# Performance work log

Measured on AMD Instinct MI355X. Metric: run time of the kernel, lower is better.

Reference implementation:

```python
import jax, jax.numpy as jnp
import numpy as np

# Model dims (GatedAttentionLayer of Qwen3.5 ANE hybrid stack)
C = 2048      # hidden_size
H = 16        # num_attention_heads
HK = 4        # num_key_value_heads
D = 128       # head_dim
ROT = 32      # rotary_dim = head_dim * partial_rotary_factor (0.25)
S = 1024      # sequence length (prefill)
CTX = 1024    # kv cache context length
N_ATTN = 6    # number of full-attention layers -> kv_cache leading dim 2*N_ATTN
EPS = 1e-6
ROPE_THETA = 1e7


def _rotate_half(x):
    h = x.shape[-1] // 2
    return jnp.concatenate([-x[..., h:], x[..., :h]], axis=-1)


def _rms_norm(x, w, eps=EPS):
    # Qwen3.5 convention: stored weight is (w - 1), applied as (1 + weight)
    r = jax.lax.rsqrt(jnp.mean(x * x, axis=-1, keepdims=True) + eps)
    return x * r * (1.0 + w)


def setup_inputs() -> dict:
    key = jax.random.key(0)
    ks = jax.random.split(key, 6)
    hidden_states = jax.random.normal(ks[0], (1, C, 1, S), jnp.float32)
    q_proj_w = jax.random.normal(ks[1], (H * 2 * D, C), jnp.float32) * 0.02  # q + gate
    k_proj_w = jax.random.normal(ks[2], (HK * D, C), jnp.float32) * 0.02
    v_proj_w = jax.random.normal(ks[3], (HK * D, C), jnp.float32) * 0.02
    o_proj_w = jax.random.normal(ks[4], (C, H * D), jnp.float32) * 0.02
    q_norm_w = jnp.zeros((D,), jnp.float32)
    k_norm_w = jnp.zeros((D,), jnp.float32)
    kv_cache = jnp.zeros((2 * N_ATTN, HK, CTX, D), jnp.float32)
    position_ids = jnp.arange(S, dtype=jnp.int32)
    # causal mask: 0 on/below diagonal, -1e9 above
    causal_mask = jnp.where(
        jnp.arange(CTX)[None, :] <= jnp.arange(S)[:, None], 0.0, -1e9
    ).astype(jnp.float32)[None, None]  # [1,1,S,CTX]
    # RoPE tables over rotary_dim
    inv_freq = 1.0 / (ROPE_THETA ** (jnp.arange(0, ROT, 2, dtype=jnp.float32) / ROT))
    t = jnp.arange(CTX, dtype=jnp.float32)
    freqs = jnp.outer(t, inv_freq)          # [CTX, ROT//2]
    emb = jnp.concatenate([freqs, freqs], -1)  # [CTX, ROT]
    cos_cached = jnp.cos(emb)
    sin_cached = jnp.sin(emb)
    return dict(hidden_states=hidden_states, q_proj_w=q_proj_w, k_proj_w=k_proj_w,
                v_proj_w=v_proj_w, o_proj_w=o_proj_w, q_norm_w=q_norm_w,
                k_norm_w=k_norm_w, kv_cache=kv_cache, causal_mask=causal_mask,
                position_ids=position_ids, cos_cached=cos_cached,
                sin_cached=sin_cached, attn_layer_idx=0)


def reference(hidden_states, q_proj_w, k_proj_w, v_proj_w, o_proj_w,
              q_norm_w, k_norm_w, kv_cache, causal_mask, position_ids,
              cos_cached, sin_cached, attn_layer_idx):
    x = hidden_states[0, :, 0, :]                     # [C, S]
    q_raw = q_proj_w @ x                              # [H*2D, S]  (1x1 Conv2d == GEMM)
    qg = q_raw.reshape(H, 2 * D, S)
    q = jnp.transpose(qg[:, :D, :], (0, 2, 1))        # [H, S, D]
    gate = jnp.transpose(qg[:, D:, :], (0, 2, 1))     # [H, S, D]
    k = jnp.transpose((k_proj_w @ x).reshape(HK, D, S), (0, 2, 1))  # [HK, S, D]
    v = jnp.transpose((v_proj_w @ x).reshape(HK, D, S), (0, 2, 1))  # [HK, S, D]

    q = _rms_norm(q, q_norm_w)
    k = _rms_norm(k, k_norm_w)

    cos = cos_cached[position_ids]   # [S, ROT]
    sin = sin_cached[position_ids]

    def rope(t):
        rot, pas = t[..., :ROT], t[..., ROT:]
        rot = rot * cos + _rotate_half(rot) * sin
        return jnp.concatenate([rot, pas], axis=-1)

    q, k = rope(q), rope(k)

    # prefill cache write at pos_start = position_ids[0]
    k_idx = 2 * attn_layer_idx
    v_idx = k_idx + 1
    pos_start = position_ids[0]
    kv_cache = jax.lax.dynamic_update_slice(kv_cache, k[None], (k_idx, 0, pos_start, 0))
    kv_cache = jax.lax.dynamic_update_slice(kv_cache, v[None], (v_idx, 0, pos_start, 0))

    g = H // HK  # GQA repeat (expand+reshape == contiguous repeat)
    k_full = jnp.repeat(kv_cache[k_idx], g, axis=0)   # [H, CTX, D]
    v_full = jnp.repeat(kv_cache[v_idx], g, axis=0)   # [H, CTX, D]

    scale = D ** -0.5
    attn = jnp.einsum('hsd,htd->hst', q, k_full) * scale + causal_mask[0]
    attn = jax.nn.softmax(attn, axis=-1)
    out = jnp.einsum('hst,htd->hsd', attn, v_full)    # [H, S, D]
    out = out * jax.nn.sigmoid(gate)
    out = jnp.transpose(out, (0, 2, 1)).reshape(H * D, S)
    output = (o_proj_w @ out)[None, :, None, :]       # [1, C, 1, S]
    return output
```

## Files before the change

### kernel.cpp

```cpp
#include <hip/hip_runtime.h>
#include <cstdint>

#define S_LEN 1024
#define C_DIM 2048
#define NH    16
#define NHK   4
#define HD    128
#define ROT   32
#define SCALE 0.08838834764831845f

typedef __bf16 bf16x8 __attribute__((ext_vector_type(8)));
typedef float floatx4 __attribute__((ext_vector_type(4)));
typedef float floatx16 __attribute__((ext_vector_type(16)));
typedef unsigned short ushortx8 __attribute__((ext_vector_type(8)));

__device__ __forceinline__ unsigned short f2bf(float f) {
  union { float f; uint32_t u; } x; x.f = f;
  uint32_t r = (x.u + 0x7fffu + ((x.u >> 16) & 1u)) >> 16;
  return (unsigned short)r;
}
__device__ __forceinline__ float bf2f(unsigned short v) {
  union { uint32_t u; float f; } x; x.u = (uint32_t)v << 16; return x.f;
}

__device__ __forceinline__ void async_copy16(const unsigned short* g, unsigned short* l) {
  __builtin_amdgcn_global_load_lds(
      (const __attribute__((address_space(1))) void*)g,
      (__attribute__((address_space(3))) void*)l,
      16, 0, 0);
}

#define WAIT_VM(N) asm volatile("s_waitcnt vmcnt(" #N ")" ::: "memory")

__device__ __forceinline__ void bar_lds_only() {
  asm volatile("s_waitcnt lgkmcnt(0)" ::: "memory");
  __builtin_amdgcn_s_barrier();
}

__device__ __forceinline__ int swz8(int row) { return (row ^ (row >> 3)) & 7; }

__global__ __launch_bounds__(256)
void prep_kernel(const float* __restrict__ qw, const float* __restrict__ kw,
                 const float* __restrict__ vw, const float* __restrict__ ow,
                 unsigned short* __restrict__ wout,
                 const float* __restrict__ x, unsigned short* __restrict__ xT) {
  __shared__ float t[32][33];
  int bid = blockIdx.x;
  if (bid < 14336) {
    const int NQ = 4096 * 2048 / 4, NK = 512 * 2048 / 4, NV = 512 * 2048 / 4;
    int i = bid * 256 + threadIdx.x;
    const float* src; int j;
    if (i < NQ) { src = qw; j = i; }
    else if (i < NQ + NK) { src = kw; j = i - NQ; }
    else if (i < NQ + NK + NV) { src = vw; j = i - NQ - NK; }
    else { src = ow; j = i - NQ - NK - NV; }
    float4 v = ((const float4*)src)[j];
    ushort4 o;
    o.x = f2bf(v.x); o.y = f2bf(v.y); o.z = f2bf(v.z); o.w = f2bf(v.w);
    ((ushort4*)wout)[i] = o;
  } else {
    int b2 = bid - 14336;
    int st = b2 & 31, ct = b2 >> 5;
    int c = threadIdx.x & 31, rq = threadIdx.x >> 5;
#pragma unroll
    for (int i = 0; i < 4; ++i) {
      int r = rq + i * 8;
      t[r][c] = x[(size_t)(ct * 32 + r) * S_LEN + st * 32 + c];
    }
    __syncthreads();
#pragma unroll
    for (int i = 0; i < 4; ++i) {
      int r = rq + i * 8;
      xT[(size_t)(st * 32 + r) * C_DIM + ct * 32 + c] = f2bf(t[c][r]);
    }
  }
}

__device__ __forceinline__ void norm_rope_epi4(
    floatx16 (&acc)[2], float (*pp)[64],
    const float* __restrict__ w, const int* __restrict__ pos_ids,
    const float* __restrict__ cosc, const float* __restrict__ sinc,
    unsigned short* __restrict__ outp,
    int wave, int lane, int wm, int scol0) {
  int l31 = lane & 31, half = lane >> 5;
#pragma unroll
  for (int ni = 0; ni < 2; ++ni) {
    float s = 0.f;
#pragma unroll
    for (int reg = 0; reg < 16; ++reg) { float v = acc[ni][reg]; s += v * v; }
    s += __shfl_xor(s, 32);
    if (half == 0) pp[wave][ni * 32 + l31] = s;
  }
  __syncthreads();
#pragma unroll
  for (int ni = 0; ni < 2; ++ni) {
    int ci = ni * 32 + l31;
    float tot = pp[0][ci] + pp[1][ci] + pp[2][ci] + pp[3][ci];
    float rn = rsqrtf(tot * (1.0f / 128.0f) + 1e-6f);
    int scol = scol0 + ni * 32 + l31;
    int pos = pos_ids[scol];
    bool rope = (wm == 0);
#pragma unroll
    for (int g = 0; g < 4; ++g) {
      int dbase = wm + half * 4 + g * 8;
      ushort4 o;
#pragma unroll
      for (int rr = 0; rr < 4; ++rr) {
        int reg = g * 4 + rr;
        int d = dbase + rr;
        float v = acc[ni][reg] * rn * (1.0f + w[d]);
        if (rope) {
          float cv = cosc[pos * ROT + d], sv = sinc[pos * ROT + d];
          int d2 = (d < 16) ? d + 16 : d - 16;
          float pv = acc[ni][reg ^ 8] * rn * (1.0f + w[d2]);
          v = v * cv + ((d < 16) ? -pv : pv) * sv;
        }
        ((unsigned short*)&o)[rr] = f2bf(v);
      }
      *(ushort4*)&outp[(size_t)scol * HD + dbase] = o;
    }
  }
}

#define STAGE_QKV4(B_, KT)                                                     \
  { _Pragma("unroll")                                                          \
    for (int i = 0; i < 4; ++i) {                                              \
      int row = wm + i * 8 + sr;                                               \
      async_copy16(Ag + (size_t)row * C_DIM + (KT) + (sc ^ swz8(row)) * 8,     \
                   &Asm[B_][(wm + i * 8) * 64]);                               \
    }                                                                          \
    _Pragma("unroll")                                                          \
    for (int i = 0; i < 2; ++i) {                                              \
      int row = wave * 16 + i * 8 + sr;                                        \
      async_copy16(Bg + (size_t)row * C_DIM + (KT) + (sc ^ swz8(row)) * 8,     \
                   &Bsm[B_][(wave * 16 + i * 8) * 64]);                        \
    } }

__global__ __launch_bounds__(256, 3)
void gemm_qkv_fused(const unsigned short* __restrict__ A,
                    const unsigned short* __restrict__ BT,
                    const float* __restrict__ qw, const float* __restrict__ kw,
                    const int* __restrict__ pos_ids,
                    const float* __restrict__ cosc, const float* __restrict__ sinc,
                    unsigned short* __restrict__ qb, unsigned short* __restrict__ kbuf,
                    unsigned short* __restrict__ vTb, unsigned short* __restrict__ sgb) {
  __shared__ unsigned short Asm[2][128 * 64];
  __shared__ unsigned short Bsm[2][64 * 64];
  __shared__ float pp[4][64];
  int tid = threadIdx.x, wave = tid >> 6, lane = tid & 63;
  int l31 = lane & 31, half = lane >> 5;
  int wm = wave * 32;
  int m0 = blockIdx.x * 128, n0 = blockIdx.y * 64;
  int sr = lane >> 3, sc = lane & 7;
  const unsigned short* Ag = A + (size_t)m0 * C_DIM;
  const unsigned short* Bg = BT + (size_t)n0 * C_DIM;
  int aswz = swz8(wm + l31);
  int bswz0 = swz8(l31), bswz1 = swz8(32 + l31);
  floatx16 acc[2];
  acc[0] = (floatx16)0.f; acc[1] = (floatx16)0.f;

  STAGE_QKV4(0, 0)
  STAGE_QKV4(1, 64)

  for (int t = 0; t < 32; ++t) {
    int b = t & 1;
    if (t < 31) { WAIT_VM(6); } else { WAIT_VM(0); }
    __builtin_amdgcn_s_barrier();
#pragma unroll
    for (int kb = 0; kb < 4; ++kb) {
      int c2 = (kb << 1) | half;
      bf16x8 av  = *(const bf16x8*)&Asm[b][(wm + l31) * 64 + ((c2 ^ aswz) << 3)];
      bf16x8 b0v = *(const bf16x8*)&Bsm[b][l31 * 64 + ((c2 ^ bswz0) << 3)];
      bf16x8 b1v = *(const bf16x8*)&Bsm[b][(32 + l31) * 64 + ((c2 ^ bswz1) << 3)];
      acc[0] = __builtin_amdgcn_mfma_f32_32x32x16_bf16(av, b0v, acc[0], 0, 0, 0);
      acc[1] = __builtin_amdgcn_mfma_f32_32x32x16_bf16(av, b1v, acc[1], 0, 0, 0);
    }
    bar_lds_only();
    if (t < 30) STAGE_QKV4(b, (t + 2) * 64)
  }

  int scol0 = n0;
  int ty = blockIdx.x;
  if (ty < 32) {
    int h = ty >> 1;
    if ((ty & 1) == 0) {
      norm_rope_epi4(acc, pp, qw, pos_ids, cosc, sinc,
                     qb + (size_t)h * S_LEN * HD, wave, lane, wm, scol0);
    } else {
#pragma unroll
      for (int ni = 0; ni < 2; ++ni) {
        int scol = scol0 + ni * 32 + l31;
#pragma unroll
        for (int g = 0; g < 4; ++g) {
          int dbase = wm + half * 4 + g * 8;
          ushort4 o;
#pragma unroll
          for (int rr = 0; rr < 4; ++rr)
            ((unsigned short*)&o)[rr] = f2bf(1.0f / (1.0f + __expf(-acc[ni][g * 4 + rr])));
          *(ushort4*)&sgb[((size_t)h * S_LEN + scol) * HD + dbase] = o;
        }
      }
    }
  } else if (ty < 36) {
    int hk = ty - 32;
    norm_rope_epi4(acc, pp, kw, pos_ids, cosc, sinc,
                   kbuf + (size_t)hk * S_LEN * HD, wave, lane, wm, scol0);
  } else {
    int hk = ty - 36;
#pragma unroll
    for (int ni = 0; ni < 2; ++ni)
#pragma unroll
      for (int reg = 0; reg < 16; ++reg) {
        int d = wm + (reg & 3) + 8 * (reg >> 2) + 4 * half;
        vTb[(size_t)hk * HD * S_LEN + (size_t)d * S_LEN + scol0 + ni * 32 + l31] =
            f2bf(acc[ni][reg]);
      }
  }
}

#define GEMM512_CORE(EXTRA_LB)                                                     \
  int tid = threadIdx.x, wave = tid >> 6, lane = tid & 63;                         \
  int l31 = lane & 31, half = lane >> 5;                                           \
  int wm = (wave & 3) * 32, wn = (wave >> 2) * 32;                                 \
  int m0 = blockIdx.x * 128, n0 = blockIdx.y * 64;                                 \
  int r8 = tid >> 3, c8 = tid & 7;                                                 \
  int arow1 = r8 + 64;                                                             \
  int apos0 = c8 ^ swz8(r8), apos1 = c8 ^ swz8(arow1), bpos = apos0;               \
  int aswz = swz8(wm + l31), bswz = swz8(wn + l31);                                \
  const unsigned short* Ag = A + (size_t)m0 * C_DIM;                               \
  const unsigned short* Bg = BT + (size_t)n0 * C_DIM;                              \
  floatx16 acc = (floatx16)0.f;                                                    \
  ushortx8 rA0, rA1, rB;                                                           \
  rA0 = *(const ushortx8*)(Ag + (size_t)r8 * C_DIM + c8 * 8);                      \
  rA1 = *(const ushortx8*)(Ag + (size_t)arow1 * C_DIM + c8 * 8);                   \
  rB  = *(const ushortx8*)(Bg + (size_t)r8 * C_DIM + c8 * 8);                      \
  *(ushortx8*)&Asm[0][r8 * 64 + apos0 * 8] = rA0;                                  \
  *(ushortx8*)&Asm[0][arow1 * 64 + apos1 * 8] = rA1;                               \
  *(ushortx8*)&Bsm[0][r8 * 64 + bpos * 8] = rB;                                    \
  bar_lds_only();                                                                  \
  for (int t = 0; t < 32; ++t) {                                                   \
    int b = t & 1;                                                                 \
    if (t < 31) {                                                                  \
      int kt = (t + 1) * 64;                                                       \
      rA0 = *(const ushortx8*)(Ag + (size_t)r8 * C_DIM + kt + c8 * 8);             \
      rA1 = *(const ushortx8*)(Ag + (size_t)arow1 * C_DIM + kt + c8 * 8);          \
      rB  = *(const ushortx8*)(Bg + (size_t)r8 * C_DIM + kt + c8 * 8);             \
    }                                                                              \
    _Pragma("unroll")                                                              \
    for (int kb = 0; kb < 4; ++kb) {                                               \
      int ca = (((kb << 1) | half) ^ aswz) << 3;                                   \
      int cb = (((kb << 1) | half) ^ bswz) << 3;                                   \
      bf16x8 av = *(const bf16x8*)&Asm[b][(wm + l31) * 64 + ca];                   \
      bf16x8 bv = *(const bf16x8*)&Bsm[b][(wn + l31) * 64 + cb];                   \
      acc = __builtin_amdgcn_mfma_f32_32x32x16_bf16(av, bv, acc, 0, 0, 0);         \
    }                                                                              \
    if (t < 31) {                                                                  \
      *(ushortx8*)&Asm[b ^ 1][r8 * 64 + apos0 * 8] = rA0;                          \
      *(ushortx8*)&Asm[b ^ 1][arow1 * 64 + apos1 * 8] = rA1;                       \
      *(ushortx8*)&Bsm[b ^ 1][r8 * 64 + bpos * 8] = rB;                            \
    }                                                                              \
    bar_lds_only();                                                                \
  }

__global__ __launch_bounds__(512, 6)
void gemm_oproj(const unsigned short* __restrict__ A,
                const unsigned short* __restrict__ BT,
                float* __restrict__ C) {
  __shared__ unsigned short Asm[2][128 * 64];
  __shared__ unsigned short Bsm[2][64 * 64];
  GEMM512_CORE()

#pragma unroll
  for (int reg = 0; reg < 16; ++reg) {
    int row = m0 + wm + (reg & 3) + 8 * (reg >> 2) + 4 * half;
    C[(size_t)row * S_LEN + n0 + wn + l31] = acc[reg];
  }
}

__global__ __launch_bounds__(256)
void attn_kernel(const unsigned short* __restrict__ qb,
                 const unsigned short* __restrict__ kbuf,
                 const unsigned short* __restrict__ vTb,
                 float* __restrict__ pm, float* __restrict__ pl,
                 float* __restrict__ pO0, float* __restrict__ pO1) {
  __shared__ __align__(16) unsigned short Ks[64 * 128];
  __shared__ __align__(16) unsigned short Vs[128 * 64];
  __shared__ __align__(16) unsigned short Ps[4][16][72];
  int h = blockIdx.x, qt = blockIdx.y, ch = blockIdx.z;
  int t0 = ch * 4;
  if (t0 > qt) return;
  int t1 = min(qt, t0 + 3);
  int s0 = qt * 64;
  int hk = h >> 2;
  int tid = threadIdx.x, wave = tid >> 6, lane = tid & 63;
  int l16 = lane & 15, quad = lane >> 4;
  int lsw = l16 & 7;

  const unsigned short* qg = qb + ((size_t)(h * S_LEN + s0 + wave * 16 + l16)) * HD;
  bf16x8 qfr[4];
#pragma unroll
  for (int kb = 0; kb < 4; ++kb)
    qfr[kb] = *(const bf16x8*)(qg + kb * 32 + quad * 8);

  float m_r[4], l_r[4];
#pragma unroll
  for (int r = 0; r < 4; ++r) { m_r[r] = -1e30f; l_r[r] = 0.f; }
  floatx4 acc_o[8];
#pragma unroll
  for (int i = 0; i < 8; ++i) acc_o[i] = (floatx4)0.f;
  int srow_base = s0 + wave * 16 + quad * 4;

  const unsigned short* kg0 = kbuf + (size_t)hk * S_LEN * HD;
  const unsigned short* vg0 = vTb + (size_t)hk * HD * S_LEN;

  int kr4 = lane >> 4, kc16 = lane & 15;
  int vr8 = lane >> 3, vc8 = lane & 7;

  for (int t = t0; t <= t1; ++t) {
    int jt = t * 64;
#pragma unroll
    for (int i = 0; i < 4; ++i) {
      int rbase = wave * 16 + i * 4;
      int row = rbase + kr4;
      int cs = kc16 ^ (row & 7);
      async_copy16(kg0 + (size_t)(jt + row) * HD + cs * 8, Ks + rbase * 128);
    }
#pragma unroll
    for (int i = 0; i < 4; ++i) {
      int rbase = wave * 32 + i * 8;
      int row = rbase + vr8;
      int cs = vc8 ^ (row & 7);
      async_copy16(vg0 + (size_t)row * S_LEN + jt + cs * 8, Vs + rbase * 64);
    }
    __syncthreads();

    floatx4 acc_s[4];
#pragma unroll
    for (int ni = 0; ni < 4; ++ni) acc_s[ni] = (floatx4)0.f;
#pragma unroll
    for (int kb = 0; kb < 4; ++kb) {
#pragma unroll
      for (int ni = 0; ni < 4; ++ni) {
        int cl = (kb * 4 + quad) ^ lsw;
        bf16x8 bk = *(const bf16x8*)&Ks[(ni * 16 + l16) * 128 + cl * 8];
        acc_s[ni] = __builtin_amdgcn_mfma_f32_16x16x32_bf16(qfr[kb], bk, acc_s[ni], 0, 0, 0);
      }
    }

    bool diag = (t == qt);
    float alpha[4];
#pragma unroll
    for (int r = 0; r < 4; ++r) {
      float scv[4];
      float mx = -1e30f;
#pragma unroll
      for (int ni = 0; ni < 4; ++ni) {
        float sv = acc_s[ni][r] * SCALE;
        if (diag) {
          int jg = jt + ni * 16 + l16;
          if (jg > srow_base + r) sv = -1e30f;
        }
        scv[ni] = sv;
        mx = fmaxf(mx, sv);
      }
#pragma unroll
      for (int off = 8; off; off >>= 1) mx = fmaxf(mx, __shfl_xor(mx, off, 16));
      float mnew = fmaxf(m_r[r], mx);
      float psv = 0.f;
#pragma unroll
      for (int ni = 0; ni < 4; ++ni) {
        float pv = (scv[ni] > -1e29f) ? __expf(scv[ni] - mnew) : 0.f;
        Ps[wave][quad * 4 + r][ni * 16 + l16] = f2bf(pv);
        psv += pv;
      }
#pragma unroll
      for (int off = 8; off; off >>= 1) psv += __shfl_xor(psv, off, 16);
      alpha[r] = __expf(m_r[r] - mnew);
      m_r[r] = mnew;
      l_r[r] = l_r[r] * alpha[r] + psv;
    }
#pragma unroll
    for (int i = 0; i < 8; ++i)
#pragma unroll
      for (int r = 0; r < 4; ++r) acc_o[i][r] *= alpha[r];
    __threadfence_block();

#pragma unroll
    for (int kb2 = 0; kb2 < 2; ++kb2) {
      bf16x8 ap = *(const bf16x8*)&Ps[wave][l16][kb2 * 32 + quad * 8];
#pragma unroll
      for (int ni2 = 0; ni2 < 8; ++ni2) {
        int cl = (kb2 * 4 + quad) ^ lsw;
        bf16x8 bv = *(const bf16x8*)&Vs[(ni2 * 16 + l16) * 64 + cl * 8];
        acc_o[ni2] = __builtin_amdgcn_mfma_f32_16x16x32_bf16(ap, bv, acc_o[ni2], 0, 0, 0);
      }
    }
    __syncthreads();
  }

  size_t pmbase = ((size_t)(h * 16 + qt) * 4 + ch) * 64;
  float* pOp = (ch < 2) ? pO0 + ((size_t)(h * 16 + qt) * 2 + ch) * 8192
                        : pO1 + ((size_t)(h * 16 + qt) * 2 + (ch - 2)) * 8192;
#pragma unroll
  for (int r = 0; r < 4; ++r) {
    int rrow = wave * 16 + quad * 4 + r;
    if (l16 == 0) { pm[pmbase + rrow] = m_r[r]; pl[pmbase + rrow] = l_r[r]; }
#pragma unroll
    for (int ni2 = 0; ni2 < 8; ++ni2)
      pOp[rrow * 128 + ni2 * 16 + l16] = acc_o[ni2][r];
  }
}

__global__ __launch_bounds__(256)
void attn_merge(const float* __restrict__ pm, const float* __restrict__ pl,
                const float* __restrict__ pO0, const float* __restrict__ pO1,
                const unsigned short* __restrict__ sgb,
                unsigned short* __restrict__ outT) {
  int h = blockIdx.x, qt = blockIdx.y;
  int vc = (qt >> 2) + 1;
  size_t base = (size_t)(h * 16 + qt) * 4;
  int lane32 = threadIdx.x & 31, rb = threadIdx.x >> 5;
  int d = lane32 * 4;
#pragma unroll
  for (int rr = 0; rr < 8; ++rr) {
    int row = rr * 8 + rb;
    float M = -1e30f;
    for (int c = 0; c < vc; ++c) M = fmaxf(M, pm[(base + c) * 64 + row]);
    float L = 0.f;
    floatx4 acc = (floatx4)0.f;
    for (int c = 0; c < vc; ++c) {
      float w = __expf(pm[(base + c) * 64 + row] - M);
      L += w * pl[(base + c) * 64 + row];
      const float* Op = (c < 2) ? pO0 + ((size_t)(h * 16 + qt) * 2 + c) * 8192
                                : pO1 + ((size_t)(h * 16 + qt) * 2 + (c - 2)) * 8192;
      floatx4 o = *(const floatx4*)&Op[row * 128 + d];
#pragma unroll
      for (int j = 0; j < 4; ++j) acc[j] += w * o[j];
    }
    float inv = 1.0f / L;
    int s = qt * 64 + row;
    ushort4 sg4 = *(const ushort4*)&sgb[((size_t)h * S_LEN + s) * HD + d];
    ushort4 out4;
#pragma unroll
    for (int j = 0; j < 4; ++j)
      ((unsigned short*)&out4)[j] = f2bf(acc[j] * inv * bf2f(((unsigned short*)&sg4)[j]));
    *(ushort4*)&outT[(size_t)s * (NH * HD) + h * HD + d] = out4;
  }
}

extern "C" void kernel_launch(void* const* d_in, const int* in_sizes, int n_in,
                              void* d_out, int out_size, void* d_ws, size_t ws_size,
                              hipStream_t stream) {
  const float* hs       = (const float*)d_in[0];
  const float* q_proj_w = (const float*)d_in[1];
  const float* k_proj_w = (const float*)d_in[2];
  const float* v_proj_w = (const float*)d_in[3];
  const float* o_proj_w = (const float*)d_in[4];
  const float* q_norm_w = (const float*)d_in[5];
  const float* k_norm_w = (const float*)d_in[6];
  const int*   pos_ids  = (const int*)d_in[9];
  const float* cos_c    = (const float*)d_in[10];
  const float* sin_c    = (const float*)d_in[11];
  float* out = (float*)d_out;

  char* ws = (char*)d_ws;
  unsigned short* wqkv = (unsigned short*)(ws + 0);
  unsigned short* wo   = (unsigned short*)(ws + 20971520);
  unsigned short* xT   = (unsigned short*)(ws + 29360128);
  unsigned short* qb   = (unsigned short*)(ws + 33554432);
  unsigned short* kbuf = (unsigned short*)(ws + 37748736);
  unsigned short* vTb  = (unsigned short*)(ws + 38797312);
  unsigned short* sgb  = (unsigned short*)(ws + 39845888);
  unsigned short* aoT  = (unsigned short*)(ws + 44040192);
  float*          pO0  = (float*)(ws + 0);
  float*          pO1  = (float*)(ws + 48234496);
  float*          pm   = (float*)(ws + 65011712);
  float*          pl   = (float*)(ws + 65273856);

  prep_kernel<<<14336 + 2048, 256, 0, stream>>>(q_proj_w, k_proj_w, v_proj_w, o_proj_w,
                                                wqkv, hs, xT);
  gemm_qkv_fused<<<dim3(40, 16), 256, 0, stream>>>(wqkv, xT, q_norm_w, k_norm_w,
                                                   pos_ids, cos_c, sin_c,
                                                   qb, kbuf, vTb, sgb);
  attn_kernel<<<dim3(16, 16, 4), 256, 0, stream>>>(qb, kbuf, vTb, pm, pl, pO0, pO1);
  attn_merge<<<dim3(16, 16), 256, 0, stream>>>(pm, pl, pO0, pO1, sgb, aoT);
  gemm_oproj<<<dim3(16, 16), 512, 0, stream>>>(wo, aoT, out);
}
```

Before: 232.7 us.

## Triple-buffer LDS in QKV and o_proj GEMMs with async copies

Both GEMMs move from double to triple LDS buffering. Each now issues the next-next stage's async copy right after the barrier, before the MFMAs run, which removes one barrier per iteration and overlaps loads with compute. The o_proj GEMM also switches from register-staged global loads to direct async global-to-LDS copies. The larger shared-memory footprint lowers occupancy (launch bounds drop to 2 blocks/CU), so latency hiding now depends on the deeper pipeline rather than on more resident waves.

```diff
diff --git a/kernel.cpp b/kernel.cpp
--- a/kernel.cpp
+++ b/kernel.cpp
@@ -136,7 +136,7 @@
                    &Bsm[B_][(wave * 16 + i * 8) * 64]);                        \
     } }
 
-__global__ __launch_bounds__(256, 3)
+__global__ __launch_bounds__(256, 2)
 void gemm_qkv_fused(const unsigned short* __restrict__ A,
                     const unsigned short* __restrict__ BT,
                     const float* __restrict__ qw, const float* __restrict__ kw,
@@ -144,8 +144,8 @@
                     const float* __restrict__ cosc, const float* __restrict__ sinc,
                     unsigned short* __restrict__ qb, unsigned short* __restrict__ kbuf,
                     unsigned short* __restrict__ vTb, unsigned short* __restrict__ sgb) {
-  __shared__ unsigned short Asm[2][128 * 64];
-  __shared__ unsigned short Bsm[2][64 * 64];
+  __shared__ unsigned short Asm[3][128 * 64];
+  __shared__ unsigned short Bsm[3][64 * 64];
   __shared__ float pp[4][64];
   int tid = threadIdx.x, wave = tid >> 6, lane = tid & 63;
   int l31 = lane & 31, half = lane >> 5;
@@ -162,10 +162,14 @@
   STAGE_QKV4(0, 0)
   STAGE_QKV4(1, 64)
 
+  int b = 0;
   for (int t = 0; t < 32; ++t) {
-    int b = t & 1;
     if (t < 31) { WAIT_VM(6); } else { WAIT_VM(0); }
-    __builtin_amdgcn_s_barrier();
+    bar_lds_only();
+    if (t < 30) {
+      int bs = b + 2; if (bs >= 3) bs -= 3;
+      STAGE_QKV4(bs, (t + 2) * 64)
+    }
 #pragma unroll
     for (int kb = 0; kb < 4; ++kb) {
       int c2 = (kb << 1) | half;
@@ -175,8 +179,7 @@
       acc[0] = __builtin_amdgcn_mfma_f32_32x32x16_bf16(av, b0v, acc[0], 0, 0, 0);
       acc[1] = __builtin_amdgcn_mfma_f32_32x32x16_bf16(av, b1v, acc[1], 0, 0, 0);
     }
-    bar_lds_only();
-    if (t < 30) STAGE_QKV4(b, (t + 2) * 64)
+    ++b; if (b >= 3) b = 0;
   }
 
   int scol0 = n0;
@@ -218,57 +221,54 @@
   }
 }
 
-#define GEMM512_CORE(EXTRA_LB)                                                     \
-  int tid = threadIdx.x, wave = tid >> 6, lane = tid & 63;                         \
-  int l31 = lane & 31, half = lane >> 5;                                           \
-  int wm = (wave & 3) * 32, wn = (wave >> 2) * 32;                                 \
-  int m0 = blockIdx.x * 128, n0 = blockIdx.y * 64;                                 \
-  int r8 = tid >> 3, c8 = tid & 7;                                                 \
-  int arow1 = r8 + 64;                                                             \
-  int apos0 = c8 ^ swz8(r8), apos1 = c8 ^ swz8(arow1), bpos = apos0;               \
-  int aswz = swz8(wm + l31), bswz = swz8(wn + l31);                                \
-  const unsigned short* Ag = A + (size_t)m0 * C_DIM;                               \
-  const unsigned short* Bg = BT + (size_t)n0 * C_DIM;                              \
-  floatx16 acc = (floatx16)0.f;                                                    \
-  ushortx8 rA0, rA1, rB;                                                           \
-  rA0 = *(const ushortx8*)(Ag + (size_t)r8 * C_DIM + c8 * 8);                      \
-  rA1 = *(const ushortx8*)(Ag + (size_t)arow1 * C_DIM + c8 * 8);                   \
-  rB  = *(const ushortx8*)(Bg + (size_t)r8 * C_DIM + c8 * 8);                      \
-  *(ushortx8*)&Asm[0][r8 * 64 + apos0 * 8] = rA0;                                  \
-  *(ushortx8*)&Asm[0][arow1 * 64 + apos1 * 8] = rA1;                               \
-  *(ushortx8*)&Bsm[0][r8 * 64 + bpos * 8] = rB;                                    \
-  bar_lds_only();                                                                  \
-  for (int t = 0; t < 32; ++t) {                                                   \
-    int b = t & 1;                                                                 \
-    if (t < 31) {                                                                  \
-      int kt = (t + 1) * 64;                                                       \
-      rA0 = *(const ushortx8*)(Ag + (size_t)r8 * C_DIM + kt + c8 * 8);             \
-      rA1 = *(const ushortx8*)(Ag + (size_t)arow1 * C_DIM + kt + c8 * 8);          \
-      rB  = *(const ushortx8*)(Bg + (size_t)r8 * C_DIM + kt + c8 * 8);             \
-    }                                                                              \
-    _Pragma("unroll")                                                              \
-    for (int kb = 0; kb < 4; ++kb) {                                               \
-      int ca = (((kb << 1) | half) ^ aswz) << 3;                                   \
-      int cb = (((kb << 1) | half) ^ bswz) << 3;                                   \
-      bf16x8 av = *(const bf16x8*)&Asm[b][(wm + l31) * 64 + ca];                   \
-      bf16x8 bv = *(const bf16x8*)&Bsm[b][(wn + l31) * 64 + cb];                   \
-      acc = __builtin_amdgcn_mfma_f32_32x32x16_bf16(av, bv, acc, 0, 0, 0);         \
-    }                                                                              \
-    if (t < 31) {                                                                  \
-      *(ushortx8*)&Asm[b ^ 1][r8 * 64 + apos0 * 8] = rA0;                          \
-      *(ushortx8*)&Asm[b ^ 1][arow1 * 64 + apos1 * 8] = rA1;                       \
-      *(ushortx8*)&Bsm[b ^ 1][r8 * 64 + bpos * 8] = rB;                            \
-    }                                                                              \
-    bar_lds_only();                                                                \
-  }
-
-__global__ __launch_bounds__(512, 6)
+#define STAGE_O8(B_, KT)                                                       \
+  { int rowA0 = r8;                                                            \
+    async_copy16(Ag + (size_t)rowA0 * C_DIM + (KT) + (c8 ^ swz8(rowA0)) * 8,   \
+                 &Asm[B_][(wave * 8) * 64]);                                   \
+    int rowA1 = r8 + 64;                                                       \
+    async_copy16(Ag + (size_t)rowA1 * C_DIM + (KT) + (c8 ^ swz8(rowA1)) * 8,   \
+                 &Asm[B_][(64 + wave * 8) * 64]);                              \
+    int rowB = r8;                                                             \
+    async_copy16(Bg + (size_t)rowB * C_DIM + (KT) + (c8 ^ swz8(rowB)) * 8,     \
+                 &Bsm[B_][(wave * 8) * 64]); }
+
+__global__ __launch_bounds__(512, 2)
 void gemm_oproj(const unsigned short* __restrict__ A,
                 const unsigned short* __restrict__ BT,
                 float* __restrict__ C) {
-  __shared__ unsigned short Asm[2][128 * 64];
-  __shared__ unsigned short Bsm[2][64 * 64];
-  GEMM512_CORE()
+  __shared__ unsigned short Asm[3][128 * 64];
+  __shared__ unsigned short Bsm[3][64 * 64];
+  int tid = threadIdx.x, wave = tid >> 6, lane = tid & 63;
+  int l31 = lane & 31, half = lane >> 5;
+  int wm = (wave & 3) * 32, wn = (wave >> 2) * 32;
+  int m0 = blockIdx.x * 128, n0 = blockIdx.y * 64;
+  int r8 = tid >> 3, c8 = tid & 7;
+  int aswz = swz8(wm + l31), bswz = swz8(wn + l31);
+  const unsigned short* Ag = A + (size_t)m0 * C_DIM;
+  const unsigned short* Bg = BT + (size_t)n0 * C_DIM;
+  floatx16 acc = (floatx16)0.f;
+
+  STAGE_O8(0, 0)
+  STAGE_O8(1, 64)
+
+  int b = 0;
+  for (int t = 0; t < 32; ++t) {
+    if (t < 31) { WAIT_VM(3); } else { WAIT_VM(0); }
+    bar_lds_only();
+    if (t < 30) {
+      int bs = b + 2; if (bs >= 3) bs -= 3;
+      STAGE_O8(bs, (t + 2) * 64)
+    }
+#pragma unroll
+    for (int kb = 0; kb < 4; ++kb) {
+      int ca = (((kb << 1) | half) ^ aswz) << 3;
+      int cb = (((kb << 1) | half) ^ bswz) << 3;
+      bf16x8 av = *(const bf16x8*)&Asm[b][(wm + l31) * 64 + ca];
+      bf16x8 bv = *(const bf16x8*)&Bsm[b][(wn + l31) * 64 + cb];
+      acc = __builtin_amdgcn_mfma_f32_32x32x16_bf16(av, bv, acc, 0, 0, 0);
+    }
+    ++b; if (b >= 3) b = 0;
+  }
 
 #pragma unroll
   for (int reg = 0; reg < 16; ++reg) {
```

After: 266.7 us. 1.15x slower.
